# Optimization experiments

Hardware: AMD Instinct MI355X
Metric: run time of the kernel (lower is better)

## Reference

```python
import jax, jax.numpy as jnp
import numpy as np

N = 100000   # nodes
E = 1600000  # edges
F = 128      # input node features
H = 128      # hidden channels
G = 512      # graphs in batch
EPS = 1e-5   # BatchNorm eps


def setup_inputs() -> dict:
    key = jax.random.key(0)
    ks = jax.random.split(key, 24)
    x = jax.random.normal(ks[0], (N, F), jnp.float32)
    edge_index = jax.random.randint(ks[1], (2, E), 0, N)
    batch = jnp.sort(jax.random.randint(ks[2], (N,), 0, G))

    def lin_w(k, i, o):
        return jax.random.normal(k, (i, o), jnp.float32) / np.sqrt(i)

    inp = {
        "x": x, "edge_index": edge_index, "batch": batch,
        "W1": lin_w(ks[3], F, H), "b1": jnp.zeros((H,), jnp.float32),
        "g1": jnp.ones((H,), jnp.float32), "be1": jnp.zeros((H,), jnp.float32),
        "m1": 0.1 * jax.random.normal(ks[4], (H,), jnp.float32),
        "v1": jax.random.uniform(ks[5], (H,), jnp.float32) + 0.5,
        "W2": lin_w(ks[6], H, H), "b2": jnp.zeros((H,), jnp.float32),
        "g2": jnp.ones((H,), jnp.float32), "be2": jnp.zeros((H,), jnp.float32),
        "m2": 0.1 * jax.random.normal(ks[7], (H,), jnp.float32),
        "v2": jax.random.uniform(ks[8], (H,), jnp.float32) + 0.5,
        "W3": lin_w(ks[9], H, H), "b3": jnp.zeros((H,), jnp.float32),
        "g3": jnp.ones((H,), jnp.float32), "be3": jnp.zeros((H,), jnp.float32),
        "m3": 0.1 * jax.random.normal(ks[10], (H,), jnp.float32),
        "v3": jax.random.uniform(ks[11], (H,), jnp.float32) + 0.5,
        "Wl": lin_w(ks[12], H, 1), "bl": jnp.zeros((1,), jnp.float32),
    }
    return inp


def _gcn_norm(edge_index):
    # add self-loops, then symmetric normalization deg^-1/2 A_hat deg^-1/2
    loops = jnp.arange(N)
    src = jnp.concatenate([edge_index[0], loops])
    dst = jnp.concatenate([edge_index[1], loops])
    deg = jax.ops.segment_sum(jnp.ones_like(src, jnp.float32), dst, num_segments=N)
    dinv = jax.lax.rsqrt(jnp.maximum(deg, 1.0))
    norm = dinv[src] * dinv[dst]  # [E+N]
    return src, dst, norm


def _gcn_conv(x, W, b, src, dst, norm):
    h = x @ W                                    # [N,H] dense GEMM first (PyG order)
    msg = h[src] * norm[:, None]                 # gather + scale, [E+N,H]
    agg = jax.ops.segment_sum(msg, dst, num_segments=N)  # scatter-add
    return agg + b


def _bn_relu(x, g, be, m, v):
    # inference BatchNorm1d (running stats) + ReLU
    return jax.nn.relu((x - m) * jax.lax.rsqrt(v + EPS) * g + be)


def reference(x, edge_index, batch,
              W1, b1, g1, be1, m1, v1,
              W2, b2, g2, be2, m2, v2,
              W3, b3, g3, be3, m3, v3,
              Wl, bl):
    src, dst, norm = _gcn_norm(edge_index)
    h = _bn_relu(_gcn_conv(x, W1, b1, src, dst, norm), g1, be1, m1, v1)
    h = _bn_relu(_gcn_conv(h, W2, b2, src, dst, norm), g2, be2, m2, v2)
    h = _bn_relu(_gcn_conv(h, W3, b3, src, dst, norm), g3, be3, m3, v3)
    # global mean pool over graphs
    sums = jax.ops.segment_sum(h, batch, num_segments=G)           # [G,H]
    cnt = jax.ops.segment_sum(jnp.ones((N,), jnp.float32), batch, num_segments=G)
    pooled = sums / jnp.maximum(cnt, 1.0)[:, None]
    # dropout is identity at inference; final linear
    return pooled @ Wl + bl  # [G,1]
```

## Files before the change

### kernel.cpp

```cpp
#include <hip/hip_runtime.h>
#include <hip/hip_bf16.h>

#define NN 100000
#define NE 1600000
#define HD 128
#define NG 512
#define BN_EPS 1e-5f

#define GEMM_BLOCKS 1563
#define HIST_BLOCKS 6250

typedef __attribute__((ext_vector_type(8))) short short8;
typedef __attribute__((ext_vector_type(4))) float floatx4;

__device__ __forceinline__ ushort f2bf(float f) {
    union { float f; uint u; } v; v.f = f;
    uint r = (v.u + 0x7FFF + ((v.u >> 16) & 1)) >> 16;
    return (ushort)r;
}
__device__ __forceinline__ float bflo(uint u) { union { uint u; float f; } v; v.u = u << 16; return v.f; }
__device__ __forceinline__ float bfhi(uint u) { union { uint u; float f; } v; v.u = u & 0xFFFF0000u; return v.f; }

__global__ void k_zero_i(int* p, int n) {
    int i = blockIdx.x * 256 + threadIdx.x;
    if (i < n) p[i] = 0;
}

__global__ void k_prep_w3(const float* __restrict__ W1, const float* __restrict__ W2,
                          const float* __restrict__ W3,
                          ushort* __restrict__ Wt1, ushort* __restrict__ Wt2,
                          ushort* __restrict__ Wt3) {
    int w = blockIdx.x >> 6;
    int i = (blockIdx.x & 63) * 256 + threadIdx.x;
    const float* W = (w == 0) ? W1 : (w == 1) ? W2 : W3;
    ushort* Wt = (w == 0) ? Wt1 : (w == 1) ? Wt2 : Wt3;
    int k = i >> 7, n = i & 127;
    Wt[n * 128 + k] = f2bf(W[i]);
}

__launch_bounds__(256)
__global__ void k_fused1(const float* __restrict__ x, const ushort* __restrict__ Wt,
                         ushort* __restrict__ hs,
                         const int* __restrict__ dst, int* __restrict__ indeg,
                         int* __restrict__ rank) {
    const int tid = threadIdx.x;
    if (blockIdx.x >= GEMM_BLOCKS) {
        int e = (blockIdx.x - GEMM_BLOCKS) * 256 + tid;
        if (e < NE) rank[e] = atomicAdd(&indeg[dst[e]], 1);
        return;
    }
    const int wave = tid >> 6, lane = tid & 63;
    const int m = lane & 15, kg = lane >> 4;
    const long row0 = (long)blockIdx.x * 64 + wave * 16;

    long arow = row0 + m;
    long arc = arow < NN ? arow : (NN - 1);
    const float* xf = x + arc * 128;
    short8 a[4];
#pragma unroll
    for (int s = 0; s < 4; ++s) {
        float4 f0 = *(const float4*)(xf + s * 32 + kg * 8);
        float4 f1 = *(const float4*)(xf + s * 32 + kg * 8 + 4);
        short8 t;
        t[0] = (short)f2bf(f0.x); t[1] = (short)f2bf(f0.y);
        t[2] = (short)f2bf(f0.z); t[3] = (short)f2bf(f0.w);
        t[4] = (short)f2bf(f1.x); t[5] = (short)f2bf(f1.y);
        t[6] = (short)f2bf(f1.z); t[7] = (short)f2bf(f1.w);
        a[s] = t;
    }

    floatx4 acc[8];
#pragma unroll
    for (int ct = 0; ct < 8; ++ct) acc[ct] = (floatx4){0.f, 0.f, 0.f, 0.f};

#pragma unroll
    for (int s = 0; s < 4; ++s) {
#pragma unroll
        for (int ct = 0; ct < 8; ++ct) {
            short8 b = *(const short8*)(Wt + (ct * 16 + m) * 128 + s * 32 + kg * 8);
            acc[ct] = __builtin_amdgcn_mfma_f32_16x16x32_bf16(a[s], b, acc[ct], 0, 0, 0);
        }
    }

#pragma unroll
    for (int r = 0; r < 4; ++r) {
        long orow = row0 + kg * 4 + r;
        if (orow < NN) {
#pragma unroll
            for (int ct = 0; ct < 8; ++ct)
                hs[orow * 128 + ct * 16 + m] = f2bf(acc[ct][r]);
        }
    }
}

__global__ void k_scan1d(const int* __restrict__ indeg, int* __restrict__ rs,
                         int* __restrict__ aux, float* __restrict__ dinv) {
    __shared__ int s[256];
    int t = threadIdx.x;
    int base = blockIdx.x * 1024 + t * 4;
    int v0 = 0, v1 = 0, v2 = 0, v3 = 0;
    if (base + 0 < NN) v0 = indeg[base + 0];
    if (base + 1 < NN) v1 = indeg[base + 1];
    if (base + 2 < NN) v2 = indeg[base + 2];
    if (base + 3 < NN) v3 = indeg[base + 3];
    if (base + 0 < NN) dinv[base + 0] = rsqrtf((float)(v0 + 1));
    if (base + 1 < NN) dinv[base + 1] = rsqrtf((float)(v1 + 1));
    if (base + 2 < NN) dinv[base + 2] = rsqrtf((float)(v2 + 1));
    if (base + 3 < NN) dinv[base + 3] = rsqrtf((float)(v3 + 1));
    int tsum = v0 + v1 + v2 + v3;
    s[t] = tsum;
    __syncthreads();
    for (int o = 1; o < 256; o <<= 1) {
        int x = 0;
        if (t >= o) x = s[t - o];
        __syncthreads();
        s[t] += x;
        __syncthreads();
    }
    int excl = s[t] - tsum;
    if (base + 0 < NN) rs[base + 0] = excl;
    if (base + 1 < NN) rs[base + 1] = excl + v0;
    if (base + 2 < NN) rs[base + 2] = excl + v0 + v1;
    if (base + 3 < NN) rs[base + 3] = excl + v0 + v1 + v2;
    if (t == 255) aux[blockIdx.x] = s[255];
}

__global__ void k_scan2(int* __restrict__ aux, int nblk) {
    __shared__ int s[128];
    int t = threadIdx.x;
    int v = (t < nblk) ? aux[t] : 0;
    s[t] = v;
    __syncthreads();
    for (int o = 1; o < 128; o <<= 1) {
        int x = 0;
        if (t >= o) x = s[t - o];
        __syncthreads();
        s[t] += x;
        __syncthreads();
    }
    if (t < nblk) aux[t] = s[t] - v;
}

__global__ void k_scan3(int* __restrict__ rs, const int* __restrict__ aux) {
    int i = blockIdx.x * 256 + threadIdx.x;
    if (i < NN) rs[i] += aux[i >> 10];
    if (i == 0) rs[NN] = NE;
}

__global__ void k_fill(const int* __restrict__ src, const int* __restrict__ dst,
                       const int* __restrict__ rank, const int* __restrict__ rs,
                       int* __restrict__ csr) {
    int e = blockIdx.x * 256 + threadIdx.x;
    if (e >= NE) return;
    csr[rs[dst[e]] + rank[e]] = src[e];
}

__global__ void k_bn_prep3(const float* __restrict__ b1, const float* __restrict__ g1,
                           const float* __restrict__ be1, const float* __restrict__ m1,
                           const float* __restrict__ v1,
                           const float* __restrict__ b2, const float* __restrict__ g2,
                           const float* __restrict__ be2, const float* __restrict__ m2,
                           const float* __restrict__ v2,
                           const float* __restrict__ b3, const float* __restrict__ g3,
                           const float* __restrict__ be3, const float* __restrict__ m3,
                           const float* __restrict__ v3,
                           float* scale1, float* shift1, float* scale2, float* shift2,
                           float* scale3, float* shift3) {
    int l = blockIdx.x, f = threadIdx.x;
    const float *b, *g, *be, *m, *v;
    float *sc, *sh;
    if (l == 0)      { b = b1; g = g1; be = be1; m = m1; v = v1; sc = scale1; sh = shift1; }
    else if (l == 1) { b = b2; g = g2; be = be2; m = m2; v = v2; sc = scale2; sh = shift2; }
    else             { b = b3; g = g3; be = be3; m = m3; v = v3; sc = scale3; sh = shift3; }
    float s = g[f] * rsqrtf(v[f] + BN_EPS);
    sc[f] = s;
    sh[f] = (b[f] - m[f]) * s + be[f];
}

__global__ void k_gstart(const int* __restrict__ batch, int* __restrict__ gstart) {
    int g = blockIdx.x * 256 + threadIdx.x;
    if (g > NG) return;
    if (g == NG) { gstart[NG] = NN; return; }
    int lo = 0, hi = NN;
    while (lo < hi) {
        int mid = (lo + hi) >> 1;
        if (batch[mid] < g) lo = mid + 1; else hi = mid;
    }
    gstart[g] = lo;
}

#define WT_STRIDE 136
__launch_bounds__(256)
__global__ void k_gemm_l23(const ushort* __restrict__ xb, const ushort* __restrict__ Wt,
                           const float* __restrict__ dinv, ushort* __restrict__ hs) {
    __shared__ ushort sWt[128 * WT_STRIDE];
    const int tid = threadIdx.x;
    for (int i = tid; i < 2048; i += 256) {
        int row = i >> 4, seg = i & 15;
        *(uint4*)&sWt[row * WT_STRIDE + seg * 8] = *(const uint4*)(Wt + row * 128 + seg * 8);
    }
    __syncthreads();

    const int wave = tid >> 6, lane = tid & 63;
    const int m = lane & 15, kg = lane >> 4;
    const long row0 = (long)blockIdx.x * 64 + wave * 16;

    long arow = row0 + m;
    long arc = arow < NN ? arow : (NN - 1);
    short8 a[4];
#pragma unroll
    for (int s = 0; s < 4; ++s)
        a[s] = *(const short8*)(xb + arc * 128 + s * 32 + kg * 8);

    floatx4 acc[8];
#pragma unroll
    for (int ct = 0; ct < 8; ++ct) acc[ct] = (floatx4){0.f, 0.f, 0.f, 0.f};

#pragma unroll
    for (int s = 0; s < 4; ++s) {
#pragma unroll
        for (int ct = 0; ct < 8; ++ct) {
            short8 b = *(const short8*)&sWt[(ct * 16 + m) * WT_STRIDE + s * 32 + kg * 8];
            acc[ct] = __builtin_amdgcn_mfma_f32_16x16x32_bf16(a[s], b, acc[ct], 0, 0, 0);
        }
    }

#pragma unroll
    for (int r = 0; r < 4; ++r) {
        long orow = row0 + kg * 4 + r;
        if (orow < NN) {
            float dd = dinv[orow];
#pragma unroll
            for (int ct = 0; ct < 8; ++ct)
                hs[orow * 128 + ct * 16 + m] = f2bf(acc[ct][r] * dd);
        }
    }
}

template <bool SCALE_SRC>
__global__ void k_gather_bf(const ushort* __restrict__ hs, const int* __restrict__ rs,
                            const int* __restrict__ csr, const float* __restrict__ dinv,
                            const float* __restrict__ scale, const float* __restrict__ shift,
                            ushort* __restrict__ xout) {
    int t = blockIdx.x * 256 + threadIdx.x;
    int d = t >> 4;
    if (d >= NN) return;
    int lane = t & 15;
    int c0 = lane * 8;
    int e0 = rs[d], e1 = rs[d + 1];
    float dd = dinv[d];

    uint4 sv = *(const uint4*)(hs + (long)d * 128 + c0);
    float w = SCALE_SRC ? dd : 1.0f;
    float a0 = w * bflo(sv.x), a1 = w * bfhi(sv.x), a2 = w * bflo(sv.y), a3 = w * bfhi(sv.y);
    float a4 = w * bflo(sv.z), a5 = w * bfhi(sv.z), a6 = w * bflo(sv.w), a7 = w * bfhi(sv.w);

    int j = e0;
    for (; j + 1 < e1; j += 2) {
        int s0 = csr[j], s1 = csr[j + 1];
        uint4 v0 = *(const uint4*)(hs + (long)s0 * 128 + c0);
        uint4 v1 = *(const uint4*)(hs + (long)s1 * 128 + c0);
        if (SCALE_SRC) {
            float w0 = dinv[s0], w1 = dinv[s1];
            a0 += w0 * bflo(v0.x) + w1 * bflo(v1.x);
            a1 += w0 * bfhi(v0.x) + w1 * bfhi(v1.x);
            a2 += w0 * bflo(v0.y) + w1 * bflo(v1.y);
            a3 += w0 * bfhi(v0.y) + w1 * bfhi(v1.y);
            a4 += w0 * bflo(v0.z) + w1 * bflo(v1.z);
            a5 += w0 * bfhi(v0.z) + w1 * bfhi(v1.z);
            a6 += w0 * bflo(v0.w) + w1 * bflo(v1.w);
            a7 += w0 * bfhi(v0.w) + w1 * bfhi(v1.w);
        } else {
            a0 += bflo(v0.x) + bflo(v1.x); a1 += bfhi(v0.x) + bfhi(v1.x);
            a2 += bflo(v0.y) + bflo(v1.y); a3 += bfhi(v0.y) + bfhi(v1.y);
            a4 += bflo(v0.z) + bflo(v1.z); a5 += bfhi(v0.z) + bfhi(v1.z);
            a6 += bflo(v0.w) + bflo(v1.w); a7 += bfhi(v0.w) + bfhi(v1.w);
        }
    }
    if (j < e1) {
        int s0 = csr[j];
        uint4 v0 = *(const uint4*)(hs + (long)s0 * 128 + c0);
        float w0 = SCALE_SRC ? dinv[s0] : 1.0f;
        a0 += w0 * bflo(v0.x); a1 += w0 * bfhi(v0.x);
        a2 += w0 * bflo(v0.y); a3 += w0 * bfhi(v0.y);
        a4 += w0 * bflo(v0.z); a5 += w0 * bfhi(v0.z);
        a6 += w0 * bflo(v0.w); a7 += w0 * bfhi(v0.w);
    }

    float4 sca = *(const float4*)(scale + c0);
    float4 scb = *(const float4*)(scale + c0 + 4);
    float4 sha = *(const float4*)(shift + c0);
    float4 shb = *(const float4*)(shift + c0 + 4);
    float r0 = fmaxf(dd * a0 * sca.x + sha.x, 0.f);
    float r1 = fmaxf(dd * a1 * sca.y + sha.y, 0.f);
    float r2 = fmaxf(dd * a2 * sca.z + sha.z, 0.f);
    float r3 = fmaxf(dd * a3 * sca.w + sha.w, 0.f);
    float r4 = fmaxf(dd * a4 * scb.x + shb.x, 0.f);
    float r5 = fmaxf(dd * a5 * scb.y + shb.y, 0.f);
    float r6 = fmaxf(dd * a6 * scb.z + shb.z, 0.f);
    float r7 = fmaxf(dd * a7 * scb.w + shb.w, 0.f);
    uint4 o;
    o.x = (uint)f2bf(r0) | ((uint)f2bf(r1) << 16);
    o.y = (uint)f2bf(r2) | ((uint)f2bf(r3) << 16);
    o.z = (uint)f2bf(r4) | ((uint)f2bf(r5) << 16);
    o.w = (uint)f2bf(r6) | ((uint)f2bf(r7) << 16);
    *(uint4*)(xout + (long)d * 128 + c0) = o;
}

__global__ void k_pool_final2(const ushort* __restrict__ x, const int* __restrict__ gstart,
                              const float* __restrict__ Wl, const float* __restrict__ bl,
                              float* __restrict__ out) {
    __shared__ float red[256];
    int g = blockIdx.x;
    int tid = threadIdx.x;
    int f = tid & 127;
    int half = tid >> 7;
    int i0 = gstart[g], i1 = gstart[g + 1];

    float acc = 0.f;
    for (int i = i0 + half; i < i1; i += 2) {
        union { uint u; float f; } v; v.u = (uint)x[(long)i * 128 + f] << 16;
        acc += v.f;
    }
    red[tid] = acc;
    __syncthreads();
    if (tid < 128) red[tid] = (red[tid] + red[tid + 128]) * Wl[tid];
    __syncthreads();
    for (int o = 64; o > 0; o >>= 1) {
        if (tid < o) red[tid] += red[tid + o];
        __syncthreads();
    }
    if (tid == 0) out[g] = red[0] / fmaxf((float)(i1 - i0), 1.f) + bl[0];
}

extern "C" void kernel_launch(void* const* d_in, const int* in_sizes, int n_in,
                              void* d_out, int out_size, void* d_ws, size_t ws_size,
                              hipStream_t stream) {
    const float* x   = (const float*)d_in[0];
    const int*   ei  = (const int*)d_in[1];
    const int*   bat = (const int*)d_in[2];
    const float* W1  = (const float*)d_in[3];
    const float* b1  = (const float*)d_in[4];
    const float* g1  = (const float*)d_in[5];
    const float* be1 = (const float*)d_in[6];
    const float* m1  = (const float*)d_in[7];
    const float* v1  = (const float*)d_in[8];
    const float* W2  = (const float*)d_in[9];
    const float* b2  = (const float*)d_in[10];
    const float* g2  = (const float*)d_in[11];
    const float* be2 = (const float*)d_in[12];
    const float* m2  = (const float*)d_in[13];
    const float* v2  = (const float*)d_in[14];
    const float* W3  = (const float*)d_in[15];
    const float* b3  = (const float*)d_in[16];
    const float* g3  = (const float*)d_in[17];
    const float* be3 = (const float*)d_in[18];
    const float* m3  = (const float*)d_in[19];
    const float* v3  = (const float*)d_in[20];
    const float* Wl  = (const float*)d_in[21];
    const float* bl  = (const float*)d_in[22];
    float* out = (float*)d_out;

    const int* srcp = ei;
    const int* dstp = ei + NE;

    char* ws = (char*)d_ws;
    size_t off = 0;
    auto alloc = [&](size_t bytes) { char* p = ws + off; off += (bytes + 255) & ~255ULL; return p; };
    float*  dinv   = (float*) alloc(NN * 4);
    int*    indeg  = (int*)   alloc(NN * 4);
    int*    rs     = (int*)   alloc((NN + 1) * 4);
    int*    aux    = (int*)   alloc(128 * 4);
    int*    csr    = (int*)   alloc(NE * 4);
    int*    rank   = (int*)   alloc(NE * 4);
    float*  scale1 = (float*) alloc(HD * 4);
    float*  shift1 = (float*) alloc(HD * 4);
    float*  scale2 = (float*) alloc(HD * 4);
    float*  shift2 = (float*) alloc(HD * 4);
    float*  scale3 = (float*) alloc(HD * 4);
    float*  shift3 = (float*) alloc(HD * 4);
    int*    gstart = (int*)   alloc((NG + 1) * 4);
    ushort* Wt1    = (ushort*)alloc(128 * 128 * 2);
    ushort* Wt2    = (ushort*)alloc(128 * 128 * 2);
    ushort* Wt3    = (ushort*)alloc(128 * 128 * 2);
    ushort* hs     = (ushort*)alloc((size_t)NN * HD * 2);
    ushort* xbuf   = (ushort*)alloc((size_t)NN * HD * 2);

    const int nblk_scan = (NN + 1023) / 1024;
    const int grid_n    = (NN + 255) / 256;
    const int grid_e    = (NE + 255) / 256;
    const int gath_grid = (NN * 16 + 255) / 256;

    k_zero_i<<<grid_n, 256, 0, stream>>>(indeg, NN);
    k_prep_w3<<<192, 256, 0, stream>>>(W1, W2, W3, Wt1, Wt2, Wt3);

    k_fused1<<<GEMM_BLOCKS + HIST_BLOCKS, 256, 0, stream>>>(x, Wt1, hs, dstp, indeg, rank);

    k_scan1d<<<nblk_scan, 256, 0, stream>>>(indeg, rs, aux, dinv);
    k_scan2<<<1, 128, 0, stream>>>(aux, nblk_scan);
    k_scan3<<<grid_n, 256, 0, stream>>>(rs, aux);
    k_fill<<<grid_e, 256, 0, stream>>>(srcp, dstp, rank, rs, csr);

    k_bn_prep3<<<3, 128, 0, stream>>>(b1, g1, be1, m1, v1, b2, g2, be2, m2, v2,
                                      b3, g3, be3, m3, v3,
                                      scale1, shift1, scale2, shift2, scale3, shift3);
    k_gstart<<<3, 256, 0, stream>>>(bat, gstart);

    k_gather_bf<true><<<gath_grid, 256, 0, stream>>>(hs, rs, csr, dinv, scale1, shift1, xbuf);
    k_gemm_l23<<<GEMM_BLOCKS, 256, 0, stream>>>(xbuf, Wt2, dinv, hs);
    k_gather_bf<false><<<gath_grid, 256, 0, stream>>>(hs, rs, csr, dinv, scale2, shift2, xbuf);
    k_gemm_l23<<<GEMM_BLOCKS, 256, 0, stream>>>(xbuf, Wt3, dinv, hs);
    k_gather_bf<false><<<gath_grid, 256, 0, stream>>>(hs, rs, csr, dinv, scale3, shift3, xbuf);

    k_pool_final2<<<NG, 256, 0, stream>>>(xbuf, gstart, Wl, bl, out);
}
```

Measured before the change: 508.1 us.

## Fuse final linear into last gather, pool via atomics; split histogram kernel

The last GCN layer's gather now applies BN+ReLU, dots each node's features with Wl, reduces across 16 lanes, and atomically adds into per-graph pooled sums. This drops the bf16 xbuf write and the separate pooling kernel's re-read. The edge histogram/rank pass moves out of the fused GEMM kernel into its own kernel, with each thread handling four edges to get more atomics in flight. Float atomics make the summation order nondeterministic, and the GEMM and histogram no longer overlap within one launch.

```diff
diff --git a/kernel.cpp b/kernel.cpp
--- a/kernel.cpp
+++ b/kernel.cpp
@@ -8,7 +8,7 @@
 #define BN_EPS 1e-5f
 
 #define GEMM_BLOCKS 1563
-#define HIST_BLOCKS 6250
+#define EQUARTER 400000
 
 typedef __attribute__((ext_vector_type(8))) short short8;
 typedef __attribute__((ext_vector_type(4))) float floatx4;
@@ -20,6 +20,8 @@
 }
 __device__ __forceinline__ float bflo(uint u) { union { uint u; float f; } v; v.u = u << 16; return v.f; }
 __device__ __forceinline__ float bfhi(uint u) { union { uint u; float f; } v; v.u = u & 0xFFFF0000u; return v.f; }
+
+__device__ __forceinline__ void atomAddF(float* p, float v) { unsafeAtomicAdd(p, v); }
 
 __global__ void k_zero_i(int* p, int n) {
     int i = blockIdx.x * 256 + threadIdx.x;
@@ -38,17 +40,28 @@
     Wt[n * 128 + k] = f2bf(W[i]);
 }
 
+__global__ void k_hist_rank4(const int* __restrict__ dst, int* __restrict__ indeg,
+                             int* __restrict__ rank) {
+    int i = blockIdx.x * 256 + threadIdx.x;
+    if (i >= EQUARTER) return;
+    int d0 = dst[i];
+    int d1 = dst[i + EQUARTER];
+    int d2 = dst[i + 2 * EQUARTER];
+    int d3 = dst[i + 3 * EQUARTER];
+    int r0 = atomicAdd(&indeg[d0], 1);
+    int r1 = atomicAdd(&indeg[d1], 1);
+    int r2 = atomicAdd(&indeg[d2], 1);
+    int r3 = atomicAdd(&indeg[d3], 1);
+    rank[i] = r0;
+    rank[i + EQUARTER] = r1;
+    rank[i + 2 * EQUARTER] = r2;
+    rank[i + 3 * EQUARTER] = r3;
+}
+
 __launch_bounds__(256)
-__global__ void k_fused1(const float* __restrict__ x, const ushort* __restrict__ Wt,
-                         ushort* __restrict__ hs,
-                         const int* __restrict__ dst, int* __restrict__ indeg,
-                         int* __restrict__ rank) {
+__global__ void k_gemm1(const float* __restrict__ x, const ushort* __restrict__ Wt,
+                        ushort* __restrict__ hs) {
     const int tid = threadIdx.x;
-    if (blockIdx.x >= GEMM_BLOCKS) {
-        int e = (blockIdx.x - GEMM_BLOCKS) * 256 + tid;
-        if (e < NE) rank[e] = atomicAdd(&indeg[dst[e]], 1);
-        return;
-    }
     const int wave = tid >> 6, lane = tid & 63;
     const int m = lane & 15, kg = lane >> 4;
     const long row0 = (long)blockIdx.x * 64 + wave * 16;
@@ -177,9 +190,11 @@
     sh[f] = (b[f] - m[f]) * s + be[f];
 }
 
-__global__ void k_gstart(const int* __restrict__ batch, int* __restrict__ gstart) {
+__global__ void k_gstart(const int* __restrict__ batch, int* __restrict__ gstart,
+                         float* __restrict__ pooled) {
     int g = blockIdx.x * 256 + threadIdx.x;
     if (g > NG) return;
+    if (g < NG) pooled[g] = 0.f;
     if (g == NG) { gstart[NG] = NN; return; }
     int lo = 0, hi = NN;
     while (lo < hi) {
@@ -307,30 +322,71 @@
     *(uint4*)(xout + (long)d * 128 + c0) = o;
 }
 
-__global__ void k_pool_final2(const ushort* __restrict__ x, const int* __restrict__ gstart,
-                              const float* __restrict__ Wl, const float* __restrict__ bl,
-                              float* __restrict__ out) {
-    __shared__ float red[256];
-    int g = blockIdx.x;
-    int tid = threadIdx.x;
-    int f = tid & 127;
-    int half = tid >> 7;
-    int i0 = gstart[g], i1 = gstart[g + 1];
-
-    float acc = 0.f;
-    for (int i = i0 + half; i < i1; i += 2) {
-        union { uint u; float f; } v; v.u = (uint)x[(long)i * 128 + f] << 16;
-        acc += v.f;
-    }
-    red[tid] = acc;
-    __syncthreads();
-    if (tid < 128) red[tid] = (red[tid] + red[tid + 128]) * Wl[tid];
-    __syncthreads();
-    for (int o = 64; o > 0; o >>= 1) {
-        if (tid < o) red[tid] += red[tid + o];
-        __syncthreads();
-    }
-    if (tid == 0) out[g] = red[0] / fmaxf((float)(i1 - i0), 1.f) + bl[0];
+__global__ void k_gather_dot(const ushort* __restrict__ hs, const int* __restrict__ rs,
+                             const int* __restrict__ csr, const float* __restrict__ dinv,
+                             const float* __restrict__ scale, const float* __restrict__ shift,
+                             const float* __restrict__ Wl, const int* __restrict__ batch,
+                             float* __restrict__ pooled) {
+    int t = blockIdx.x * 256 + threadIdx.x;
+    int d = t >> 4;
+    if (d >= NN) return;
+    int lane = t & 15;
+    int c0 = lane * 8;
+    int e0 = rs[d], e1 = rs[d + 1];
+    float dd = dinv[d];
+
+    uint4 sv = *(const uint4*)(hs + (long)d * 128 + c0);
+    float a0 = bflo(sv.x), a1 = bfhi(sv.x), a2 = bflo(sv.y), a3 = bfhi(sv.y);
+    float a4 = bflo(sv.z), a5 = bfhi(sv.z), a6 = bflo(sv.w), a7 = bfhi(sv.w);
+
+    int j = e0;
+    for (; j + 1 < e1; j += 2) {
+        int s0 = csr[j], s1 = csr[j + 1];
+        uint4 v0 = *(const uint4*)(hs + (long)s0 * 128 + c0);
+        uint4 v1 = *(const uint4*)(hs + (long)s1 * 128 + c0);
+        a0 += bflo(v0.x) + bflo(v1.x); a1 += bfhi(v0.x) + bfhi(v1.x);
+        a2 += bflo(v0.y) + bflo(v1.y); a3 += bfhi(v0.y) + bfhi(v1.y);
+        a4 += bflo(v0.z) + bflo(v1.z); a5 += bfhi(v0.z) + bfhi(v1.z);
+        a6 += bflo(v0.w) + bflo(v1.w); a7 += bfhi(v0.w) + bfhi(v1.w);
+    }
+    if (j < e1) {
+        int s0 = csr[j];
+        uint4 v0 = *(const uint4*)(hs + (long)s0 * 128 + c0);
+        a0 += bflo(v0.x); a1 += bfhi(v0.x);
+        a2 += bflo(v0.y); a3 += bfhi(v0.y);
+        a4 += bflo(v0.z); a5 += bfhi(v0.z);
+        a6 += bflo(v0.w); a7 += bfhi(v0.w);
+    }
+
+    float4 sca = *(const float4*)(scale + c0);
+    float4 scb = *(const float4*)(scale + c0 + 4);
+    float4 sha = *(const float4*)(shift + c0);
+    float4 shb = *(const float4*)(shift + c0 + 4);
+    float4 wa  = *(const float4*)(Wl + c0);
+    float4 wb  = *(const float4*)(Wl + c0 + 4);
+    float sum =
+        fmaxf(dd * a0 * sca.x + sha.x, 0.f) * wa.x +
+        fmaxf(dd * a1 * sca.y + sha.y, 0.f) * wa.y +
+        fmaxf(dd * a2 * sca.z + sha.z, 0.f) * wa.z +
+        fmaxf(dd * a3 * sca.w + sha.w, 0.f) * wa.w +
+        fmaxf(dd * a4 * scb.x + shb.x, 0.f) * wb.x +
+        fmaxf(dd * a5 * scb.y + shb.y, 0.f) * wb.y +
+        fmaxf(dd * a6 * scb.z + shb.z, 0.f) * wb.z +
+        fmaxf(dd * a7 * scb.w + shb.w, 0.f) * wb.w;
+
+    sum += __shfl_down(sum, 8, 16);
+    sum += __shfl_down(sum, 4, 16);
+    sum += __shfl_down(sum, 2, 16);
+    sum += __shfl_down(sum, 1, 16);
+    if (lane == 0) atomAddF(&pooled[batch[d]], sum);
+}
+
+__global__ void k_final(const float* __restrict__ pooled, const int* __restrict__ gstart,
+                        const float* __restrict__ bl, float* __restrict__ out) {
+    int g = blockIdx.x * 256 + threadIdx.x;
+    if (g >= NG) return;
+    float c = (float)(gstart[g + 1] - gstart[g]);
+    out[g] = pooled[g] / fmaxf(c, 1.f) + bl[0];
 }
 
 extern "C" void kernel_launch(void* const* d_in, const int* in_sizes, int n_in,
@@ -380,6 +436,7 @@
     float*  scale3 = (float*) alloc(HD * 4);
     float*  shift3 = (float*) alloc(HD * 4);
     int*    gstart = (int*)   alloc((NG + 1) * 4);
+    float*  pooled = (float*) alloc(NG * 4);
     ushort* Wt1    = (ushort*)alloc(128 * 128 * 2);
     ushort* Wt2    = (ushort*)alloc(128 * 128 * 2);
     ushort* Wt3    = (ushort*)alloc(128 * 128 * 2);
@@ -389,12 +446,14 @@
     const int nblk_scan = (NN + 1023) / 1024;
     const int grid_n    = (NN + 255) / 256;
     const int grid_e    = (NE + 255) / 256;
+    const int hist_grid = (EQUARTER + 255) / 256;
     const int gath_grid = (NN * 16 + 255) / 256;
 
     k_zero_i<<<grid_n, 256, 0, stream>>>(indeg, NN);
     k_prep_w3<<<192, 256, 0, stream>>>(W1, W2, W3, Wt1, Wt2, Wt3);
 
-    k_fused1<<<GEMM_BLOCKS + HIST_BLOCKS, 256, 0, stream>>>(x, Wt1, hs, dstp, indeg, rank);
+    k_hist_rank4<<<hist_grid, 256, 0, stream>>>(dstp, indeg, rank);
+    k_gemm1<<<GEMM_BLOCKS, 256, 0, stream>>>(x, Wt1, hs);
 
     k_scan1d<<<nblk_scan, 256, 0, stream>>>(indeg, rs, aux, dinv);
     k_scan2<<<1, 128, 0, stream>>>(aux, nblk_scan);
@@ -404,13 +463,13 @@
     k_bn_prep3<<<3, 128, 0, stream>>>(b1, g1, be1, m1, v1, b2, g2, be2, m2, v2,
                                       b3, g3, be3, m3, v3,
                                       scale1, shift1, scale2, shift2, scale3, shift3);
-    k_gstart<<<3, 256, 0, stream>>>(bat, gstart);
+    k_gstart<<<3, 256, 0, stream>>>(bat, gstart, pooled);
 
     k_gather_bf<true><<<gath_grid, 256, 0, stream>>>(hs, rs, csr, dinv, scale1, shift1, xbuf);
     k_gemm_l23<<<GEMM_BLOCKS, 256, 0, stream>>>(xbuf, Wt2, dinv, hs);
     k_gather_bf<false><<<gath_grid, 256, 0, stream>>>(hs, rs, csr, dinv, scale2, shift2, xbuf);
     k_gemm_l23<<<GEMM_BLOCKS, 256, 0, stream>>>(xbuf, Wt3, dinv, hs);
-    k_gather_bf<false><<<gath_grid, 256, 0, stream>>>(hs, rs, csr, dinv, scale3, shift3, xbuf);
-
-    k_pool_final2<<<NG, 256, 0, stream>>>(xbuf, gstart, Wl, bl, out);
-}
+    k_gather_dot<<<gath_grid, 256, 0, stream>>>(hs, rs, csr, dinv, scale3, shift3, Wl, bat, pooled);
+
+    k_final<<<2, 256, 0, stream>>>(pooled, gstart, bl, out);
+}
```

Measured after the change: 646.5 us. 27.2% more time.
